# Performance work log

Measured on AMD Instinct MI355X. Metric: run time of the kernel, lower is better.

## Reference

```python
import jax, jax.numpy as jnp
import numpy as np

EPS = 1e-8


def _layer_norm(x, w, b):
    mu = jnp.mean(x, axis=-1, keepdims=True)
    var = jnp.mean((x - mu) ** 2, axis=-1, keepdims=True)
    return (x - mu) * jax.lax.rsqrt(var + EPS) * w + b


def setup_inputs() -> dict:
    key = jax.random.key(0)
    k1, k2, k3 = jax.random.split(key, 3)
    B, S, D = 8, 2048, 1024
    return {
        "x_real": jax.random.normal(k1, (B, S, D), dtype=jnp.float32),
        "x_imag": jax.random.normal(k2, (B, S, D), dtype=jnp.float32),
        "phase_matrix": jax.random.normal(k3, (D, D), dtype=jnp.float32) * 0.02,
        "coherence_factor": jnp.ones((1,), dtype=jnp.float32) * 0.1,
        "ln_weight": jnp.ones((D,), dtype=jnp.float32),
        "ln_bias": jnp.zeros((D,), dtype=jnp.float32),
    }


def reference(x_real, x_imag, phase_matrix, coherence_factor, ln_weight, ln_bias):
    D = x_real.shape[-1]
    # coherence = mean_{i,j} cos(phi_i - phi_j) over the last dim pairwise;
    # exact trig identity: sum_{i,j} cos(phi_i-phi_j) = (sum cos)^2 + (sum sin)^2
    phases = jnp.arctan2(x_imag + EPS, x_real + EPS)          # [B,S,D]
    sc = jnp.sum(jnp.cos(phases), axis=-1, keepdims=True)      # [B,S,1]
    ss = jnp.sum(jnp.sin(phases), axis=-1, keepdims=True)      # [B,S,1]
    coherence = (sc * sc + ss * ss) / (D * D)                  # [B,S,1]

    # phase rotation driven by GEMM
    phase_adjustment = jnp.einsum('bsd,de->bse', x_real, phase_matrix)
    phase_adjustment = phase_adjustment * coherence_factor * (1.0 - coherence)
    c, s = jnp.cos(phase_adjustment), jnp.sin(phase_adjustment)
    new_real = x_real * c - x_imag * s
    new_imag = x_real * s + x_imag * c

    # unit-modulus normalization
    norm = jnp.sqrt(new_real ** 2 + new_imag ** 2 + EPS)
    new_real = new_real / norm
    new_imag = new_imag / norm

    return (_layer_norm(new_real, ln_weight, ln_bias),
            _layer_norm(new_imag, ln_weight, ln_bias))
```

## Files before the change

### kernel.cpp

```cpp
#include <hip/hip_runtime.h>
#include <hip/hip_fp16.h>

#define DEV __device__ __forceinline__

typedef __bf16 bf16x8 __attribute__((ext_vector_type(8)));
typedef float f32x4 __attribute__((ext_vector_type(4)));
typedef short s16x8 __attribute__((ext_vector_type(8)));
typedef unsigned short u16;

static constexpr int D = 1024;
static constexpr int M = 16384;
static constexpr int R = 32;
static constexpr float EPS = 1e-8f;
static constexpr int PAD = 1028;

static constexpr int SMEM_BYTES = 136192;
static constexpr int B_OFF_U16 = 32768;
static constexpr int RED_OFF = 131584;
static constexpr int STATS_OFF = 135680;

DEV u16 f2bf(float f) {
  union { float f; unsigned u; } v; v.f = f;
  unsigned u = v.u;
  return (u16)((u + 0x7FFFu + ((u >> 16) & 1u)) >> 16);
}

DEV void async_copy16(const void* g, void* l) {
  __builtin_amdgcn_global_load_lds(
      (const __attribute__((address_space(1))) void*)g,
      (__attribute__((address_space(3))) void*)l, 16, 0, 0);
}

union H2x4 { s16x8 v; __half2 h[4]; };

__global__ __launch_bounds__(256) void k_prep(const float* __restrict__ pm,
                                              u16* __restrict__ bt) {
  __shared__ float t[32][33];
  int bx = blockIdx.x * 32, by = blockIdx.y * 32;
  int tx = threadIdx.x, ty = threadIdx.y;
#pragma unroll
  for (int j = 0; j < 32; j += 8)
    t[ty + j][tx] = pm[(size_t)(by + ty + j) * D + bx + tx];
  __syncthreads();
#pragma unroll
  for (int j = 0; j < 32; j += 8) {
    int col = bx + ty + j, k = by + tx;
    int kk = k >> 5, nh = col >> 9, cb = (col >> 4) & 31, c15 = col & 15;
    int kg = (k >> 3) & 3, je = k & 7;
    bt[(size_t)(kk * 2 + nh) * 16384 + (size_t)((cb * 64 + kg * 16 + c15) * 8 + je)] =
        f2bf(t[tx][ty + j]);
  }
}

__global__ __launch_bounds__(512, 2) void k_fused(
    const float* __restrict__ xr, const float* __restrict__ xi,
    const u16* __restrict__ bt, const float* __restrict__ cfp,
    const float* __restrict__ lw, const float* __restrict__ lb,
    float* __restrict__ outR, float* __restrict__ outI) {
  __shared__ __align__(16) unsigned char smem[SMEM_BYTES];
  u16* A_lds = (u16*)smem;
  u16* B_lds = (u16*)smem + B_OFF_U16;
  __half2* stash = (__half2*)smem;
  float* red = (float*)(smem + RED_OFF);
  float* stats = (float*)(smem + STATS_OFF);

  const int tid = threadIdx.x;
  const int lane = tid & 63;
  const int l15 = lane & 15, l4 = lane >> 4;
  const int wv = tid >> 6;
  const size_t row0 = (size_t)blockIdx.x * R;
  const float cfv = cfp[0];

  {
    int row = tid >> 4;
    int s16 = tid & 15;
    const float* src = xr + (row0 + row) * D;
#pragma unroll
    for (int it = 0; it < 4; ++it)
#pragma unroll
      for (int h = 0; h < 2; ++h) {
        int kgl = it * 32 + s16 * 2 + h;
        f32x4 a = *(const f32x4*)(src + kgl * 8);
        f32x4 b = *(const f32x4*)(src + kgl * 8 + 4);
        s16x8 v;
        v[0] = (short)f2bf(a.x); v[1] = (short)f2bf(a.y);
        v[2] = (short)f2bf(a.z); v[3] = (short)f2bf(a.w);
        v[4] = (short)f2bf(b.x); v[5] = (short)f2bf(b.y);
        v[6] = (short)f2bf(b.z); v[7] = (short)f2bf(b.w);
        int kk = kgl >> 2, kg = kgl & 3;
        int u = kk * 128 + (row >> 4) * 64 + kg * 16 + ((row & 15) ^ (kk & 15));
        *(s16x8*)&A_lds[u * 8] = v;
      }
  }
  __syncthreads();

  f32x4 acc[2][8] = {};

  auto stage = [&](int buf, int s) {
    const u16* src = bt + (size_t)s * 16384;
    u16* dst = &B_lds[buf * 16384];
#pragma unroll
    for (int i = 0; i < 4; ++i) {
      int off = ((wv * 4 + i) * 64 + lane) * 8;
      async_copy16(src + off, dst + off);
    }
  };

  stage(0, 0);
  asm volatile("s_waitcnt vmcnt(0)" ::: "memory");
  __builtin_amdgcn_s_barrier();

  for (int kk = 0; kk < 32; ++kk) {
    bf16x8 af[2];
#pragma unroll
    for (int rb = 0; rb < 2; ++rb) {
      int u = kk * 128 + rb * 64 + l4 * 16 + (l15 ^ (kk & 15));
      af[rb] = __builtin_bit_cast(bf16x8, *(const s16x8*)&A_lds[u * 8]);
    }
#pragma unroll
    for (int nh = 0; nh < 2; ++nh) {
      int s = kk * 2 + nh;
      if (s < 63) {
        stage((s + 1) & 1, s + 1);
        asm volatile("s_waitcnt vmcnt(4)" ::: "memory");
      } else {
        asm volatile("s_waitcnt vmcnt(0)" ::: "memory");
      }
      __builtin_amdgcn_s_barrier();
      const u16* bb = &B_lds[(s & 1) * 16384];
#pragma unroll
      for (int nf = 0; nf < 4; ++nf) {
        int u = (wv * 4 + nf) * 64 + l4 * 16 + l15;
        bf16x8 bf = __builtin_bit_cast(bf16x8, *(const s16x8*)&bb[u * 8]);
        acc[0][nh * 4 + nf] =
            __builtin_amdgcn_mfma_f32_16x16x32_bf16(af[0], bf, acc[0][nh * 4 + nf], 0, 0, 0);
        acc[1][nh * 4 + nf] =
            __builtin_amdgcn_mfma_f32_16x16x32_bf16(af[1], bf, acc[1][nh * 4 + nf], 0, 0, 0);
      }
      __builtin_amdgcn_s_barrier();
    }
  }
  __syncthreads();

  float sc8[8], ss8[8];
#pragma unroll
  for (int p = 0; p < 8; ++p) { sc8[p] = 0.f; ss8[p] = 0.f; }
#pragma unroll
  for (int rb = 0; rb < 2; ++rb)
#pragma unroll
    for (int i = 0; i < 4; ++i) {
      const int p = rb * 4 + i;
      const int row_l = rb * 16 + l4 * 4 + i;
      const float* ar = xr + (row0 + row_l) * D;
      const float* ai = xi + (row0 + row_l) * D;
#pragma unroll
      for (int q = 0; q < 8; ++q) {
        int col = (q >> 2) * 512 + wv * 64 + (q & 3) * 16 + l15;
        float a = ar[col], b = ai[col];
        float xe = a + EPS, ye = b + EPS;
        float inv = rsqrtf(xe * xe + ye * ye);
        sc8[p] += xe * inv;
        ss8[p] += ye * inv;
        stash[row_l * PAD + col] = __floats2half2_rn(a, b);
      }
    }
#pragma unroll
  for (int p = 0; p < 8; ++p)
#pragma unroll
    for (int d = 1; d < 16; d <<= 1) {
      sc8[p] += __shfl_xor(sc8[p], d, 64);
      ss8[p] += __shfl_xor(ss8[p], d, 64);
    }
  if (l15 == 0) {
#pragma unroll
    for (int rb = 0; rb < 2; ++rb)
#pragma unroll
      for (int i = 0; i < 4; ++i) {
        int p = rb * 4 + i, row_l = rb * 16 + l4 * 4 + i;
        red[(row_l * 8 + wv) * 4 + 0] = sc8[p];
        red[(row_l * 8 + wv) * 4 + 1] = ss8[p];
      }
  }
  __syncthreads();
  float srow[8];
#pragma unroll
  for (int rb = 0; rb < 2; ++rb)
#pragma unroll
    for (int i = 0; i < 4; ++i) {
      int p = rb * 4 + i, row_l = rb * 16 + l4 * 4 + i;
      float tsc = 0.f, tss = 0.f;
#pragma unroll
      for (int w8 = 0; w8 < 8; ++w8) {
        tsc += red[(row_l * 8 + w8) * 4 + 0];
        tss += red[(row_l * 8 + w8) * 4 + 1];
      }
      float coh = (tsc * tsc + tss * tss) * (1.0f / (1024.0f * 1024.0f));
      srow[p] = cfv * (1.0f - coh);
    }
  __syncthreads();

  float snr[8], sqr[8], sni[8], sqi[8];
#pragma unroll
  for (int p = 0; p < 8; ++p) { snr[p] = 0.f; sqr[p] = 0.f; sni[p] = 0.f; sqi[p] = 0.f; }
#pragma unroll
  for (int rb = 0; rb < 2; ++rb)
#pragma unroll
    for (int i = 0; i < 4; ++i) {
      const int p = rb * 4 + i;
      const int row_l = rb * 16 + l4 * 4 + i;
      const float sr = srow[p];
#pragma unroll
      for (int q = 0; q < 8; ++q) {
        int col = (q >> 2) * 512 + wv * 64 + (q & 3) * 16 + l15;
        float t = acc[rb][q][i] * sr;
        float t2 = t * t;
        float sn = t * (1.f + t2 * (-1.f / 6.f + t2 * (1.f / 120.f - t2 * (1.f / 5040.f))));
        float cs = 1.f + t2 * (-0.5f + t2 * (1.f / 24.f - t2 * (1.f / 720.f)));
        __half2 ab = stash[row_l * PAD + col];
        float a = __low2float(ab), b = __high2float(ab);
        float nr = a * cs - b * sn;
        float ni = a * sn + b * cs;
        float inv = rsqrtf(nr * nr + ni * ni + EPS);
        nr *= inv; ni *= inv;
        stash[row_l * PAD + col] = __floats2half2_rn(nr, ni);
        snr[p] += nr; sqr[p] += nr * nr;
        sni[p] += ni; sqi[p] += ni * ni;
      }
    }
#pragma unroll
  for (int p = 0; p < 8; ++p)
#pragma unroll
    for (int d = 1; d < 16; d <<= 1) {
      snr[p] += __shfl_xor(snr[p], d, 64);
      sqr[p] += __shfl_xor(sqr[p], d, 64);
      sni[p] += __shfl_xor(sni[p], d, 64);
      sqi[p] += __shfl_xor(sqi[p], d, 64);
    }
  if (l15 == 0) {
#pragma unroll
    for (int rb = 0; rb < 2; ++rb)
#pragma unroll
      for (int i = 0; i < 4; ++i) {
        int p = rb * 4 + i, row_l = rb * 16 + l4 * 4 + i;
        red[(row_l * 8 + wv) * 4 + 0] = snr[p];
        red[(row_l * 8 + wv) * 4 + 1] = sqr[p];
        red[(row_l * 8 + wv) * 4 + 2] = sni[p];
        red[(row_l * 8 + wv) * 4 + 3] = sqi[p];
      }
  }
  __syncthreads();
  if (wv == 0 && l15 == 0) {
#pragma unroll
    for (int rb = 0; rb < 2; ++rb)
#pragma unroll
      for (int i = 0; i < 4; ++i) {
        int row_l = rb * 16 + l4 * 4 + i;
        float s0 = 0.f, s1 = 0.f, s2 = 0.f, s3 = 0.f;
#pragma unroll
        for (int w8 = 0; w8 < 8; ++w8) {
          s0 += red[(row_l * 8 + w8) * 4 + 0];
          s1 += red[(row_l * 8 + w8) * 4 + 1];
          s2 += red[(row_l * 8 + w8) * 4 + 2];
          s3 += red[(row_l * 8 + w8) * 4 + 3];
        }
        float mu_r = s0 * (1.f / 1024.f);
        float mu_i = s2 * (1.f / 1024.f);
        stats[row_l * 4 + 0] = mu_r;
        stats[row_l * 4 + 1] = rsqrtf(s1 * (1.f / 1024.f) - mu_r * mu_r + EPS);
        stats[row_l * 4 + 2] = mu_i;
        stats[row_l * 4 + 3] = rsqrtf(s3 * (1.f / 1024.f) - mu_i * mu_i + EPS);
      }
  }
  __syncthreads();

  {
    int row = tid >> 4, cg = tid & 15;
    float mu_r = stats[row * 4 + 0], rd_r = stats[row * 4 + 1];
    float mu_i = stats[row * 4 + 2], rd_i = stats[row * 4 + 3];
    float* orp = outR + (row0 + row) * D;
    float* oip = outI + (row0 + row) * D;
#pragma unroll
    for (int v = 0; v < 16; ++v) {
      int col = v * 64 + cg * 4;
      H2x4 hv;
      hv.v = *(const s16x8*)&stash[row * PAD + col];
      f32x4 w4 = *(const f32x4*)(lw + col);
      f32x4 b4 = *(const f32x4*)(lb + col);
      f32x4 o_r, o_i;
#pragma unroll
      for (int j = 0; j < 4; ++j) {
        float nr = __low2float(hv.h[j]), ni = __high2float(hv.h[j]);
        o_r[j] = (nr - mu_r) * rd_r * w4[j] + b4[j];
        o_i[j] = (ni - mu_i) * rd_i * w4[j] + b4[j];
      }
      *(f32x4*)(orp + col) = o_r;
      *(f32x4*)(oip + col) = o_i;
    }
  }
}

extern "C" void kernel_launch(void* const* d_in, const int* in_sizes, int n_in,
                              void* d_out, int out_size, void* d_ws, size_t ws_size,
                              hipStream_t stream) {
  const float* xr = (const float*)d_in[0];
  const float* xi = (const float*)d_in[1];
  const float* pm = (const float*)d_in[2];
  const float* cf = (const float*)d_in[3];
  const float* lw = (const float*)d_in[4];
  const float* lb = (const float*)d_in[5];
  float* outR = (float*)d_out;
  float* outI = outR + (size_t)M * D;
  u16* bt = (u16*)d_ws;

  k_prep<<<dim3(32, 32), dim3(32, 8), 0, stream>>>(pm, bt);
  k_fused<<<M / R, 512, 0, stream>>>(xr, xi, bt, cf, lw, lb, outR, outI);
}
```

Measured before the change: 137.0 us.

## Load B fragments directly from global into registers with double buffering

Replaces the LDS-staged, barrier-synchronized B pipeline (global_load_lds into two LDS buffers) with per-wave direct global loads of B fragments into registers, double-buffered across k-steps. The goal is to remove per-step block barriers and LDS traffic for B. It also raises MFMA wave priority around compute via s_setprio. In exchange it holds more registers (16 bf16x8 B fragments) and each wave hits global/L2 without shared reuse, since every wave reads distinct B columns.

```diff
diff --git a/kernel.cpp b/kernel.cpp
--- a/kernel.cpp
+++ b/kernel.cpp
@@ -15,7 +15,6 @@
 static constexpr int PAD = 1028;
 
 static constexpr int SMEM_BYTES = 136192;
-static constexpr int B_OFF_U16 = 32768;
 static constexpr int RED_OFF = 131584;
 static constexpr int STATS_OFF = 135680;
 
@@ -23,12 +22,6 @@
   union { float f; unsigned u; } v; v.f = f;
   unsigned u = v.u;
   return (u16)((u + 0x7FFFu + ((u >> 16) & 1u)) >> 16);
-}
-
-DEV void async_copy16(const void* g, void* l) {
-  __builtin_amdgcn_global_load_lds(
-      (const __attribute__((address_space(1))) void*)g,
-      (__attribute__((address_space(3))) void*)l, 16, 0, 0);
 }
 
 union H2x4 { s16x8 v; __half2 h[4]; };
@@ -59,7 +52,6 @@
     float* __restrict__ outR, float* __restrict__ outI) {
   __shared__ __align__(16) unsigned char smem[SMEM_BYTES];
   u16* A_lds = (u16*)smem;
-  u16* B_lds = (u16*)smem + B_OFF_U16;
   __half2* stash = (__half2*)smem;
   float* red = (float*)(smem + RED_OFF);
   float* stats = (float*)(smem + STATS_OFF);
@@ -96,48 +88,40 @@
 
   f32x4 acc[2][8] = {};
 
-  auto stage = [&](int buf, int s) {
-    const u16* src = bt + (size_t)s * 16384;
-    u16* dst = &B_lds[buf * 16384];
-#pragma unroll
-    for (int i = 0; i < 4; ++i) {
-      int off = ((wv * 4 + i) * 64 + lane) * 8;
-      async_copy16(src + off, dst + off);
-    }
-  };
-
-  stage(0, 0);
-  asm volatile("s_waitcnt vmcnt(0)" ::: "memory");
-  __builtin_amdgcn_s_barrier();
-
-  for (int kk = 0; kk < 32; ++kk) {
-    bf16x8 af[2];
+  auto loadA = [&](int kk, bf16x8 (&af)[2]) {
 #pragma unroll
     for (int rb = 0; rb < 2; ++rb) {
       int u = kk * 128 + rb * 64 + l4 * 16 + (l15 ^ (kk & 15));
       af[rb] = __builtin_bit_cast(bf16x8, *(const s16x8*)&A_lds[u * 8]);
     }
-#pragma unroll
-    for (int nh = 0; nh < 2; ++nh) {
-      int s = kk * 2 + nh;
-      if (s < 63) {
-        stage((s + 1) & 1, s + 1);
-        asm volatile("s_waitcnt vmcnt(4)" ::: "memory");
-      } else {
-        asm volatile("s_waitcnt vmcnt(0)" ::: "memory");
-      }
-      __builtin_amdgcn_s_barrier();
-      const u16* bb = &B_lds[(s & 1) * 16384];
-#pragma unroll
-      for (int nf = 0; nf < 4; ++nf) {
-        int u = (wv * 4 + nf) * 64 + l4 * 16 + l15;
-        bf16x8 bf = __builtin_bit_cast(bf16x8, *(const s16x8*)&bb[u * 8]);
-        acc[0][nh * 4 + nf] =
-            __builtin_amdgcn_mfma_f32_16x16x32_bf16(af[0], bf, acc[0][nh * 4 + nf], 0, 0, 0);
-        acc[1][nh * 4 + nf] =
-            __builtin_amdgcn_mfma_f32_16x16x32_bf16(af[1], bf, acc[1][nh * 4 + nf], 0, 0, 0);
-      }
-      __builtin_amdgcn_s_barrier();
+  };
+  const u16* bwave = bt + (size_t)(wv * 4) * 512 + (size_t)lane * 8;
+  auto loadB = [&](int kk, bf16x8 (&b)[8]) {
+    const u16* p = bwave + (size_t)kk * 32768;
+#pragma unroll
+    for (int f = 0; f < 8; ++f)
+      b[f] = __builtin_bit_cast(bf16x8,
+          *(const s16x8*)(p + (f >> 2) * 16384 + (f & 3) * 512));
+  };
+  auto step = [&](bf16x8 (&af)[2], bf16x8 (&b)[8]) {
+    __builtin_amdgcn_s_setprio(1);
+#pragma unroll
+    for (int f = 0; f < 8; ++f) {
+      acc[0][f] = __builtin_amdgcn_mfma_f32_16x16x32_bf16(af[0], b[f], acc[0][f], 0, 0, 0);
+      acc[1][f] = __builtin_amdgcn_mfma_f32_16x16x32_bf16(af[1], b[f], acc[1][f], 0, 0, 0);
+    }
+    __builtin_amdgcn_s_setprio(0);
+  };
+
+  {
+    bf16x8 afA[2], afB[2], bA[8], bB[8];
+    loadA(0, afA); loadB(0, bA);
+    for (int t = 0; t < 16; ++t) {
+      int kk = t * 2;
+      loadA(kk + 1, afB); loadB(kk + 1, bB);
+      step(afA, bA);
+      if (t < 15) { loadA(kk + 2, afA); loadB(kk + 2, bA); }
+      step(afB, bB);
     }
   }
   __syncthreads();
```

Result: slower. 160.4 us (+17.1%).
